# Kernel optimization log

Hardware: AMD Instinct MI355X
Metric: run time of the kernel (lower is better)

The kernel has to match this reference:

```python
import jax, jax.numpy as jnp
import numpy as np

B, C, D = 16, 128, 256


def setup_inputs() -> dict:
    key = jax.random.key(0)
    ks = jax.random.split(key, 12)
    s = 0.05
    return {
        "h_t": jax.random.normal(ks[0], (B, C, D), jnp.float32),
        "A_a": jax.random.normal(ks[1], (C, C), jnp.float32) * s,
        "A_m": jax.random.normal(ks[2], (C, C), jnp.float32) * s,
        "W1": jax.random.normal(ks[3], (2 * D, D), jnp.float32) * s,
        "b1": jax.random.normal(ks[4], (D,), jnp.float32) * s,
        "W2": jax.random.normal(ks[5], (D, 1), jnp.float32) * s,
        "b2": jax.random.normal(ks[6], (1,), jnp.float32) * s,
        "Wa": jax.random.normal(ks[7], (D, D), jnp.float32) * s,
        "ba": jax.random.normal(ks[8], (D,), jnp.float32) * s,
        "Wm": jax.random.normal(ks[9], (D, D), jnp.float32) * s,
        "bm": jax.random.normal(ks[10], (D,), jnp.float32) * s,
        "beta1": jnp.float32(1.0),
        "beta2": jnp.float32(1.0),
        "beta3": jnp.float32(1.0),
    }


def reference(h_t, A_a, A_m, W1, b1, W2, b2, Wa, ba, Wm, bm, beta1, beta2, beta3):
    d = h_t.shape[-1]
    # Pairwise edge-MLP score S[b,u,v] = sigmoid(W2 @ relu(W1 @ [h_u; h_v] + b1) + b2).
    # Split W1 into the half acting on h_u and the half acting on h_v, so the
    # (B,C,C,2D) concat never materializes (same math as Linear on the concat).
    pre_u = jnp.einsum('bud,dk->buk', h_t, W1[:d])        # (B,C,D)
    pre_v = jnp.einsum('bvd,dk->bvk', h_t, W1[d:])        # (B,C,D)
    hidden = jax.nn.relu(pre_u[:, :, None, :] + pre_v[:, None, :, :] + b1)  # (B,C,C,D)
    S = jax.nn.sigmoid(jnp.einsum('buvk,ko->buvo', hidden, W2)[..., 0] + b2[0])  # (B,C,C)

    # Additive aggregation: a_t[b,v,:] = sum_u (S*A_a)[b,u,v] * h_t[b,u,:]
    a_t = jnp.einsum('buv,bud->bvd', S * A_a, h_t)

    # Hadamard aggregation: m_t[b,v,d] = sum_u A_m[u,v] * h[b,u,d] * h[b,v,d]
    #                              = (A_m^T @ h_t) * h_t  (avoids (B,C,C,D) tensor)
    m_t = jnp.einsum('uv,bud->bvd', A_m, h_t) * h_t

    z_t = (beta1 * h_t
           + beta2 * (jnp.einsum('bvd,de->bve', a_t, Wa) + ba)
           + beta3 * (jnp.einsum('bvd,de->bve', m_t, Wm) + bm))
    return z_t
```

## Files before the change

kernel.cpp:

```cpp
#include <hip/hip_runtime.h>
#include <hip/hip_bf16.h>

#define B_ 16
#define C_ 128
#define D_ 256

typedef unsigned int uint32;
typedef unsigned short u16;
typedef __attribute__((ext_vector_type(8))) short s8v;
typedef __attribute__((ext_vector_type(4))) float f4v;

__device__ __forceinline__ u16 bfu(float x) {
  union { __hip_bfloat16 h; u16 s; } u;
  u.h = __float2bfloat16(x);
  return u.s;
}
__device__ __forceinline__ float2 bf2x(uint32 x) {
  return make_float2(__uint_as_float(x << 16), __uint_as_float(x & 0xffff0000u));
}

__global__ __launch_bounds__(256) void kprep(const float* __restrict__ h,
    const float* __restrict__ W1, const float* __restrict__ Wa,
    const float* __restrict__ Wm, const float* __restrict__ Am,
    const float* __restrict__ ba, const float* __restrict__ bm,
    const float* __restrict__ be2, const float* __restrict__ be3,
    u16* __restrict__ hbT, u16* __restrict__ w1t,
    u16* __restrict__ wcatT, u16* __restrict__ amT, float* __restrict__ bcat) {
  const int blk = blockIdx.x;
  const int tid = threadIdx.x;
  if (blk < 512) {
    const int i4 = (blk * 256 + tid) * 4;
    const int b = i4 >> 15, r = i4 & 32767, d = r >> 7, u0 = r & 127;
    ushort4 o;
    o.x = bfu(h[(b * C_ + u0 + 0) * D_ + d]);
    o.y = bfu(h[(b * C_ + u0 + 1) * D_ + d]);
    o.z = bfu(h[(b * C_ + u0 + 2) * D_ + d]);
    o.w = bfu(h[(b * C_ + u0 + 3) * D_ + d]);
    *(ushort4*)(hbT + i4) = o;
  } else if (blk < 640) {
    const int i4 = ((blk - 512) * 256 + tid) * 4;
    const int n = i4 >> 8, k0 = i4 & 255;
    float x0, x1, x2, x3;
    if (n < 256) {
      x0 = W1[(k0 + 0) * 256 + n]; x1 = W1[(k0 + 1) * 256 + n];
      x2 = W1[(k0 + 2) * 256 + n]; x3 = W1[(k0 + 3) * 256 + n];
    } else {
      const int nn = n - 256;
      x0 = W1[(256 + k0 + 0) * 256 + nn]; x1 = W1[(256 + k0 + 1) * 256 + nn];
      x2 = W1[(256 + k0 + 2) * 256 + nn]; x3 = W1[(256 + k0 + 3) * 256 + nn];
    }
    ushort4 o; o.x = bfu(x0); o.y = bfu(x1); o.z = bfu(x2); o.w = bfu(x3);
    *(ushort4*)(w1t + i4) = o;
  } else if (blk < 768) {
    const float b2v = be2[0], b3v = be3[0];
    const int i4 = ((blk - 640) * 256 + tid) * 4;
    const int n = i4 >> 9, k0 = i4 & 511;
    float x0, x1, x2, x3;
    if (k0 < 256) {
      x0 = b2v * Wa[(k0 + 0) * 256 + n]; x1 = b2v * Wa[(k0 + 1) * 256 + n];
      x2 = b2v * Wa[(k0 + 2) * 256 + n]; x3 = b2v * Wa[(k0 + 3) * 256 + n];
    } else {
      const int kk = k0 - 256;
      x0 = b3v * Wm[(kk + 0) * 256 + n]; x1 = b3v * Wm[(kk + 1) * 256 + n];
      x2 = b3v * Wm[(kk + 2) * 256 + n]; x3 = b3v * Wm[(kk + 3) * 256 + n];
    }
    ushort4 o; o.x = bfu(x0); o.y = bfu(x1); o.z = bfu(x2); o.w = bfu(x3);
    *(ushort4*)(wcatT + i4) = o;
  } else if (blk < 784) {
    const int i4 = ((blk - 768) * 256 + tid) * 4;
    const int v = i4 >> 7, u0 = i4 & 127;
    ushort4 o;
    o.x = bfu(Am[(u0 + 0) * C_ + v]);
    o.y = bfu(Am[(u0 + 1) * C_ + v]);
    o.z = bfu(Am[(u0 + 2) * C_ + v]);
    o.w = bfu(Am[(u0 + 3) * C_ + v]);
    *(ushort4*)(amT + i4) = o;
  } else {
    bcat[tid] = be2[0] * ba[tid] + be3[0] * bm[tid];
  }
}

__global__ __launch_bounds__(256) void k1_mfma(const float* __restrict__ h,
    const u16* __restrict__ w1t, const float* __restrict__ b1,
    u16* __restrict__ P, u16* __restrict__ Q) {
  const int lane = threadIdx.x & 63;
  const int w = blockIdx.x * 4 + (threadIdx.x >> 6);
  const int nt = w & 31, mt = w >> 5;
  const int row0 = mt * 16, col0 = nt * 16;
  const int lr = lane & 15, lk = lane >> 4;
  const float* ap = h + (row0 + lr) * D_ + lk * 8;
  const u16* bp = w1t + (col0 + lr) * D_ + lk * 8;
  f4v acc = {0.f, 0.f, 0.f, 0.f};
#pragma unroll
  for (int ks = 0; ks < 8; ++ks) {
    const float4 a0 = *(const float4*)(ap + ks * 32);
    const float4 a1 = *(const float4*)(ap + ks * 32 + 4);
    union { s8v v; u16 u[8]; } af;
    af.u[0] = bfu(a0.x); af.u[1] = bfu(a0.y); af.u[2] = bfu(a0.z); af.u[3] = bfu(a0.w);
    af.u[4] = bfu(a1.x); af.u[5] = bfu(a1.y); af.u[6] = bfu(a1.z); af.u[7] = bfu(a1.w);
    const s8v bf = *(const s8v*)(bp + ks * 32);
    acc = __builtin_amdgcn_mfma_f32_16x16x32_bf16(af.v, bf, acc, 0, 0, 0);
  }
  const int col = col0 + lr;
  if (col0 < 256) {
#pragma unroll
    for (int r = 0; r < 4; ++r)
      P[(row0 + lk * 4 + r) * D_ + col] = bfu(acc[r]);
  } else {
    const float bb = b1[col - 256];
#pragma unroll
    for (int r = 0; r < 4; ++r)
      Q[(row0 + lk * 4 + r) * D_ + (col - 256)] = bfu(acc[r] + bb);
  }
}

__global__ __launch_bounds__(256) void k2_s(const u16* __restrict__ P,
    const u16* __restrict__ Q, const float* __restrict__ W2,
    const float* __restrict__ b2, const float* __restrict__ Aa,
    u16* __restrict__ SA) {
  const int b = blockIdx.z;
  const int u0 = blockIdx.x * 16;
  const int v0 = blockIdx.y * 16;
  const int tid = threadIdx.x;
  __shared__ uint32 Pl[16][130];
  __shared__ uint32 Ql[16][130];
  const uint32* Pg = (const uint32*)(P + (b * C_ + u0) * D_);
  const uint32* Qg = (const uint32*)(Q + (b * C_ + v0) * D_);
  {
    const int r = tid >> 5;
    const int c4 = (tid & 31) * 4;
#pragma unroll
    for (int half = 0; half < 2; ++half) {
      const int rr = r + half * 8;
      const uint4 pv = *(const uint4*)&Pg[rr * 128 + c4];
      const uint4 qv = *(const uint4*)&Qg[rr * 128 + c4];
      *(uint2*)&Pl[rr][c4]     = make_uint2(pv.x, pv.y);
      *(uint2*)&Pl[rr][c4 + 2] = make_uint2(pv.z, pv.w);
      *(uint2*)&Ql[rr][c4]     = make_uint2(qv.x, qv.y);
      *(uint2*)&Ql[rr][c4 + 2] = make_uint2(qv.z, qv.w);
    }
  }
  __syncthreads();
  const int ul = tid & 15;
  const int vl = tid >> 4;
  const float4* __restrict__ w4 = (const float4*)W2;
  float a0 = 0.f, a1 = 0.f;
#pragma unroll 8
  for (int kk = 0; kk < 128; kk += 2) {
    const uint2 pu = *(const uint2*)&Pl[ul][kk];
    const uint2 qu = *(const uint2*)&Ql[vl][kk];
    const float4 wv = w4[kk >> 1];
    const float2 p0 = bf2x(pu.x), p1 = bf2x(pu.y);
    const float2 q0 = bf2x(qu.x), q1 = bf2x(qu.y);
    a0 = fmaf(fmaxf(p0.x + q0.x, 0.f), wv.x, a0);
    a0 = fmaf(fmaxf(p0.y + q0.y, 0.f), wv.y, a0);
    a1 = fmaf(fmaxf(p1.x + q1.x, 0.f), wv.z, a1);
    a1 = fmaf(fmaxf(p1.y + q1.y, 0.f), wv.w, a1);
  }
  const float s = 1.f / (1.f + __expf(-(a0 + a1 + b2[0])));
  const int u = u0 + ul, v = v0 + vl;
  SA[b * C_ * C_ + v * C_ + u] = bfu(s * Aa[u * C_ + v]);
}

__global__ __launch_bounds__(512) void k34_mfma(const u16* __restrict__ SA,
    const u16* __restrict__ amT, const u16* __restrict__ hbT,
    const u16* __restrict__ wcatT, const float* __restrict__ bcat,
    const float* __restrict__ h, const float* __restrict__ be1,
    float* __restrict__ z) {
  const int bid = blockIdx.x;
  const int tid = threadIdx.x;
  const int bt = bid >> 3;
  const int v0 = (bid & 7) * 16;
  const int lane = tid & 63, widx = tid >> 6;
  const int lr = lane & 15, lk = lane >> 4;
  __shared__ u16 at[16 * 512];

#pragma unroll
  for (int i = 0; i < 2; ++i) {
    const int d0 = (widx * 2 + i) * 16;
    const u16* sap = SA + (bt * C_ + v0 + lr) * C_ + lk * 8;
    const u16* a2p = amT + (v0 + lr) * C_ + lk * 8;
    const u16* bp  = hbT + (bt * D_ + d0 + lr) * C_ + lk * 8;
    f4v acca = {0.f, 0.f, 0.f, 0.f}, accm = {0.f, 0.f, 0.f, 0.f};
#pragma unroll
    for (int ks = 0; ks < 4; ++ks) {
      const s8v a1 = *(const s8v*)(sap + ks * 32);
      const s8v a2 = *(const s8v*)(a2p + ks * 32);
      const s8v bf = *(const s8v*)(bp + ks * 32);
      acca = __builtin_amdgcn_mfma_f32_16x16x32_bf16(a1, bf, acca, 0, 0, 0);
      accm = __builtin_amdgcn_mfma_f32_16x16x32_bf16(a2, bf, accm, 0, 0, 0);
    }
    const int d = d0 + lr;
#pragma unroll
    for (int r = 0; r < 4; ++r) {
      const int R = lk * 4 + r;
      const int grow = bt * C_ + v0 + R;
      const float hv = h[grow * D_ + d];
      const int swz = (R & 7) << 4;
      *(u16*)((char*)at + R * 1024 + ((d * 2) ^ swz)) = bfu(acca[r]);
      *(u16*)((char*)at + R * 1024 + (((256 + d) * 2) ^ swz)) = bfu(accm[r] * hv);
    }
  }
  __syncthreads();

  const float b1v = be1[0];
#pragma unroll
  for (int i = 0; i < 2; ++i) {
    const int col0 = (widx * 2 + i) * 16;
    const u16* bp = wcatT + (col0 + lr) * 512 + lk * 8;
    f4v acc = {0.f, 0.f, 0.f, 0.f};
#pragma unroll
    for (int ks = 0; ks < 16; ++ks) {
      const int boff = lr * 1024 + ((ks * 64 + lk * 16) ^ ((lr & 7) << 4));
      const s8v af = *(const s8v*)((char*)at + boff);
      const s8v bf = *(const s8v*)(bp + ks * 32);
      acc = __builtin_amdgcn_mfma_f32_16x16x32_bf16(af, bf, acc, 0, 0, 0);
    }
    const int col = col0 + lr;
    const float bc = bcat[col];
#pragma unroll
    for (int r = 0; r < 4; ++r) {
      const int row = bt * C_ + v0 + lk * 4 + r;
      z[row * D_ + col] = acc[r] + b1v * h[row * D_ + col] + bc;
    }
  }
}

extern "C" void kernel_launch(void* const* d_in, const int* in_sizes, int n_in,
                              void* d_out, int out_size, void* d_ws, size_t ws_size,
                              hipStream_t stream) {
  const float* h   = (const float*)d_in[0];
  const float* Aa  = (const float*)d_in[1];
  const float* Am  = (const float*)d_in[2];
  const float* W1  = (const float*)d_in[3];
  const float* b1  = (const float*)d_in[4];
  const float* W2  = (const float*)d_in[5];
  const float* b2  = (const float*)d_in[6];
  const float* Wa  = (const float*)d_in[7];
  const float* ba  = (const float*)d_in[8];
  const float* Wm  = (const float*)d_in[9];
  const float* bm  = (const float*)d_in[10];
  const float* be1 = (const float*)d_in[11];
  const float* be2 = (const float*)d_in[12];
  const float* be3 = (const float*)d_in[13];
  float* z = (float*)d_out;

  char* wsb = (char*)d_ws;
  u16*   w1t   = (u16*)(wsb);
  u16*   wcatT = (u16*)(wsb + (256 << 10));
  u16*   amT   = (u16*)(wsb + (512 << 10));
  float* bcat  = (float*)(wsb + (544 << 10));
  u16*   hbT   = (u16*)(wsb + (1 << 20));
  u16*   P     = (u16*)(wsb + (2 << 20));
  u16*   Q     = (u16*)(wsb + (3 << 20));
  u16*   SA    = (u16*)(wsb + (4 << 20));

  kprep  <<<785,  256, 0, stream>>>(h, W1, Wa, Wm, Am, ba, bm, be2, be3,
                                    hbT, w1t, wcatT, amT, bcat);
  k1_mfma<<<1024, 256, 0, stream>>>(h, w1t, b1, P, Q);
  k2_s   <<<dim3(8, 8, 16), 256, 0, stream>>>(P, Q, W2, b2, Aa, SA);
  k34_mfma<<<128, 512, 0, stream>>>(SA, amT, hbT, wcatT, bcat, h, be1, z);
}
```

Before: 122.0 us.

## Fuse edge-MLP projections into score kernel and drop weight prep kernel

Removes the separate prep and projection kernels. P and Q are now computed per tile with MFMA inside the score kernel, writing straight to shared memory, and W1, Wa, Wm, Am and h are converted from fp32 to bf16 inline rather than pre-transposed. This saves two launches and the global round-trips for the prepped weights and P/Q. In exchange, every tile recomputes its P/Q rows (8x redundancy per batch) and reads the weights with strided scalar fp32 loads, which adds heavy L2 traffic.

```diff
diff --git a/kernel.cpp b/kernel.cpp
--- a/kernel.cpp
+++ b/kernel.cpp
@@ -19,128 +19,75 @@
   return make_float2(__uint_as_float(x << 16), __uint_as_float(x & 0xffff0000u));
 }
 
-__global__ __launch_bounds__(256) void kprep(const float* __restrict__ h,
-    const float* __restrict__ W1, const float* __restrict__ Wa,
-    const float* __restrict__ Wm, const float* __restrict__ Am,
-    const float* __restrict__ ba, const float* __restrict__ bm,
-    const float* __restrict__ be2, const float* __restrict__ be3,
-    u16* __restrict__ hbT, u16* __restrict__ w1t,
-    u16* __restrict__ wcatT, u16* __restrict__ amT, float* __restrict__ bcat) {
-  const int blk = blockIdx.x;
-  const int tid = threadIdx.x;
-  if (blk < 512) {
-    const int i4 = (blk * 256 + tid) * 4;
-    const int b = i4 >> 15, r = i4 & 32767, d = r >> 7, u0 = r & 127;
-    ushort4 o;
-    o.x = bfu(h[(b * C_ + u0 + 0) * D_ + d]);
-    o.y = bfu(h[(b * C_ + u0 + 1) * D_ + d]);
-    o.z = bfu(h[(b * C_ + u0 + 2) * D_ + d]);
-    o.w = bfu(h[(b * C_ + u0 + 3) * D_ + d]);
-    *(ushort4*)(hbT + i4) = o;
-  } else if (blk < 640) {
-    const int i4 = ((blk - 512) * 256 + tid) * 4;
-    const int n = i4 >> 8, k0 = i4 & 255;
-    float x0, x1, x2, x3;
-    if (n < 256) {
-      x0 = W1[(k0 + 0) * 256 + n]; x1 = W1[(k0 + 1) * 256 + n];
-      x2 = W1[(k0 + 2) * 256 + n]; x3 = W1[(k0 + 3) * 256 + n];
-    } else {
-      const int nn = n - 256;
-      x0 = W1[(256 + k0 + 0) * 256 + nn]; x1 = W1[(256 + k0 + 1) * 256 + nn];
-      x2 = W1[(256 + k0 + 2) * 256 + nn]; x3 = W1[(256 + k0 + 3) * 256 + nn];
-    }
-    ushort4 o; o.x = bfu(x0); o.y = bfu(x1); o.z = bfu(x2); o.w = bfu(x3);
-    *(ushort4*)(w1t + i4) = o;
-  } else if (blk < 768) {
-    const float b2v = be2[0], b3v = be3[0];
-    const int i4 = ((blk - 640) * 256 + tid) * 4;
-    const int n = i4 >> 9, k0 = i4 & 511;
-    float x0, x1, x2, x3;
-    if (k0 < 256) {
-      x0 = b2v * Wa[(k0 + 0) * 256 + n]; x1 = b2v * Wa[(k0 + 1) * 256 + n];
-      x2 = b2v * Wa[(k0 + 2) * 256 + n]; x3 = b2v * Wa[(k0 + 3) * 256 + n];
-    } else {
-      const int kk = k0 - 256;
-      x0 = b3v * Wm[(kk + 0) * 256 + n]; x1 = b3v * Wm[(kk + 1) * 256 + n];
-      x2 = b3v * Wm[(kk + 2) * 256 + n]; x3 = b3v * Wm[(kk + 3) * 256 + n];
-    }
-    ushort4 o; o.x = bfu(x0); o.y = bfu(x1); o.z = bfu(x2); o.w = bfu(x3);
-    *(ushort4*)(wcatT + i4) = o;
-  } else if (blk < 784) {
-    const int i4 = ((blk - 768) * 256 + tid) * 4;
-    const int v = i4 >> 7, u0 = i4 & 127;
-    ushort4 o;
-    o.x = bfu(Am[(u0 + 0) * C_ + v]);
-    o.y = bfu(Am[(u0 + 1) * C_ + v]);
-    o.z = bfu(Am[(u0 + 2) * C_ + v]);
-    o.w = bfu(Am[(u0 + 3) * C_ + v]);
-    *(ushort4*)(amT + i4) = o;
-  } else {
-    bcat[tid] = be2[0] * ba[tid] + be3[0] * bm[tid];
-  }
-}
-
-__global__ __launch_bounds__(256) void k1_mfma(const float* __restrict__ h,
-    const u16* __restrict__ w1t, const float* __restrict__ b1,
-    u16* __restrict__ P, u16* __restrict__ Q) {
-  const int lane = threadIdx.x & 63;
-  const int w = blockIdx.x * 4 + (threadIdx.x >> 6);
-  const int nt = w & 31, mt = w >> 5;
-  const int row0 = mt * 16, col0 = nt * 16;
-  const int lr = lane & 15, lk = lane >> 4;
-  const float* ap = h + (row0 + lr) * D_ + lk * 8;
-  const u16* bp = w1t + (col0 + lr) * D_ + lk * 8;
-  f4v acc = {0.f, 0.f, 0.f, 0.f};
-#pragma unroll
-  for (int ks = 0; ks < 8; ++ks) {
-    const float4 a0 = *(const float4*)(ap + ks * 32);
-    const float4 a1 = *(const float4*)(ap + ks * 32 + 4);
-    union { s8v v; u16 u[8]; } af;
-    af.u[0] = bfu(a0.x); af.u[1] = bfu(a0.y); af.u[2] = bfu(a0.z); af.u[3] = bfu(a0.w);
-    af.u[4] = bfu(a1.x); af.u[5] = bfu(a1.y); af.u[6] = bfu(a1.z); af.u[7] = bfu(a1.w);
-    const s8v bf = *(const s8v*)(bp + ks * 32);
-    acc = __builtin_amdgcn_mfma_f32_16x16x32_bf16(af.v, bf, acc, 0, 0, 0);
-  }
-  const int col = col0 + lr;
-  if (col0 < 256) {
-#pragma unroll
-    for (int r = 0; r < 4; ++r)
-      P[(row0 + lk * 4 + r) * D_ + col] = bfu(acc[r]);
-  } else {
-    const float bb = b1[col - 256];
-#pragma unroll
-    for (int r = 0; r < 4; ++r)
-      Q[(row0 + lk * 4 + r) * D_ + (col - 256)] = bfu(acc[r] + bb);
-  }
-}
-
-__global__ __launch_bounds__(256) void k2_s(const u16* __restrict__ P,
-    const u16* __restrict__ Q, const float* __restrict__ W2,
-    const float* __restrict__ b2, const float* __restrict__ Aa,
-    u16* __restrict__ SA) {
+__global__ __launch_bounds__(256) void k12(const float* __restrict__ h,
+    const float* __restrict__ W1, const float* __restrict__ b1,
+    const float* __restrict__ W2, const float* __restrict__ b2,
+    const float* __restrict__ Aa, u16* __restrict__ SA) {
   const int b = blockIdx.z;
   const int u0 = blockIdx.x * 16;
   const int v0 = blockIdx.y * 16;
   const int tid = threadIdx.x;
+  const int lane = tid & 63;
+  const int widx = tid >> 6;
+  const int lr = lane & 15, lk = lane >> 4;
   __shared__ uint32 Pl[16][130];
   __shared__ uint32 Ql[16][130];
-  const uint32* Pg = (const uint32*)(P + (b * C_ + u0) * D_);
-  const uint32* Qg = (const uint32*)(Q + (b * C_ + v0) * D_);
-  {
-    const int r = tid >> 5;
-    const int c4 = (tid & 31) * 4;
-#pragma unroll
-    for (int half = 0; half < 2; ++half) {
-      const int rr = r + half * 8;
-      const uint4 pv = *(const uint4*)&Pg[rr * 128 + c4];
-      const uint4 qv = *(const uint4*)&Qg[rr * 128 + c4];
-      *(uint2*)&Pl[rr][c4]     = make_uint2(pv.x, pv.y);
-      *(uint2*)&Pl[rr][c4 + 2] = make_uint2(pv.z, pv.w);
-      *(uint2*)&Ql[rr][c4]     = make_uint2(qv.x, qv.y);
-      *(uint2*)&Ql[rr][c4 + 2] = make_uint2(qv.z, qv.w);
-    }
+  u16* PlH = (u16*)&Pl[0][0];
+  u16* QlH = (u16*)&Ql[0][0];
+
+  const float* apP = h + (b * C_ + u0 + lr) * D_ + lk * 8;
+  const float* apQ = h + (b * C_ + v0 + lr) * D_ + lk * 8;
+  s8v aP[8], aQ[8];
+#pragma unroll
+  for (int ks = 0; ks < 8; ++ks) {
+    const float4 x0 = *(const float4*)(apP + ks * 32);
+    const float4 x1 = *(const float4*)(apP + ks * 32 + 4);
+    const float4 y0 = *(const float4*)(apQ + ks * 32);
+    const float4 y1 = *(const float4*)(apQ + ks * 32 + 4);
+    union { s8v v; u16 u[8]; } t, s;
+    t.u[0] = bfu(x0.x); t.u[1] = bfu(x0.y); t.u[2] = bfu(x0.z); t.u[3] = bfu(x0.w);
+    t.u[4] = bfu(x1.x); t.u[5] = bfu(x1.y); t.u[6] = bfu(x1.z); t.u[7] = bfu(x1.w);
+    s.u[0] = bfu(y0.x); s.u[1] = bfu(y0.y); s.u[2] = bfu(y0.z); s.u[3] = bfu(y0.w);
+    s.u[4] = bfu(y1.x); s.u[5] = bfu(y1.y); s.u[6] = bfu(y1.z); s.u[7] = bfu(y1.w);
+    aP[ks] = t.v;
+    aQ[ks] = s.v;
+  }
+
+#pragma unroll
+  for (int i = 0; i < 4; ++i) {
+    const int n = (widx * 4 + i) * 16 + lr;
+    f4v acc = {0.f, 0.f, 0.f, 0.f};
+#pragma unroll
+    for (int ks = 0; ks < 8; ++ks) {
+      union { s8v v; u16 u[8]; } bf;
+#pragma unroll
+      for (int j = 0; j < 8; ++j)
+        bf.u[j] = bfu(W1[(ks * 32 + lk * 8 + j) * D_ + n]);
+      acc = __builtin_amdgcn_mfma_f32_16x16x32_bf16(aP[ks], bf.v, acc, 0, 0, 0);
+    }
+#pragma unroll
+    for (int r = 0; r < 4; ++r)
+      PlH[(lk * 4 + r) * 260 + n] = bfu(acc[r]);
+  }
+#pragma unroll
+  for (int i = 0; i < 4; ++i) {
+    const int n = (widx * 4 + i) * 16 + lr;
+    f4v acc = {0.f, 0.f, 0.f, 0.f};
+#pragma unroll
+    for (int ks = 0; ks < 8; ++ks) {
+      union { s8v v; u16 u[8]; } bf;
+#pragma unroll
+      for (int j = 0; j < 8; ++j)
+        bf.u[j] = bfu(W1[(D_ + ks * 32 + lk * 8 + j) * D_ + n]);
+      acc = __builtin_amdgcn_mfma_f32_16x16x32_bf16(aQ[ks], bf.v, acc, 0, 0, 0);
+    }
+    const float bb = b1[n];
+#pragma unroll
+    for (int r = 0; r < 4; ++r)
+      QlH[(lk * 4 + r) * 260 + n] = bfu(acc[r] + bb);
   }
   __syncthreads();
+
   const int ul = tid & 15;
   const int vl = tid >> 4;
   const float4* __restrict__ w4 = (const float4*)W2;
@@ -162,11 +109,12 @@
   SA[b * C_ * C_ + v * C_ + u] = bfu(s * Aa[u * C_ + v]);
 }
 
-__global__ __launch_bounds__(512) void k34_mfma(const u16* __restrict__ SA,
-    const u16* __restrict__ amT, const u16* __restrict__ hbT,
-    const u16* __restrict__ wcatT, const float* __restrict__ bcat,
-    const float* __restrict__ h, const float* __restrict__ be1,
-    float* __restrict__ z) {
+__global__ __launch_bounds__(512) void k34(const u16* __restrict__ SA,
+    const float* __restrict__ Am, const float* __restrict__ h,
+    const float* __restrict__ Wa, const float* __restrict__ Wm,
+    const float* __restrict__ ba, const float* __restrict__ bm,
+    const float* __restrict__ be1, const float* __restrict__ be2,
+    const float* __restrict__ be3, float* __restrict__ z) {
   const int bid = blockIdx.x;
   const int tid = threadIdx.x;
   const int bt = bid >> 3;
@@ -174,23 +122,27 @@
   const int lane = tid & 63, widx = tid >> 6;
   const int lr = lane & 15, lk = lane >> 4;
   __shared__ u16 at[16 * 512];
+  const float b2v = be2[0], b3v = be3[0];
 
 #pragma unroll
   for (int i = 0; i < 2; ++i) {
     const int d0 = (widx * 2 + i) * 16;
+    const int d = d0 + lr;
     const u16* sap = SA + (bt * C_ + v0 + lr) * C_ + lk * 8;
-    const u16* a2p = amT + (v0 + lr) * C_ + lk * 8;
-    const u16* bp  = hbT + (bt * D_ + d0 + lr) * C_ + lk * 8;
     f4v acca = {0.f, 0.f, 0.f, 0.f}, accm = {0.f, 0.f, 0.f, 0.f};
 #pragma unroll
     for (int ks = 0; ks < 4; ++ks) {
       const s8v a1 = *(const s8v*)(sap + ks * 32);
-      const s8v a2 = *(const s8v*)(a2p + ks * 32);
-      const s8v bf = *(const s8v*)(bp + ks * 32);
-      acca = __builtin_amdgcn_mfma_f32_16x16x32_bf16(a1, bf, acca, 0, 0, 0);
-      accm = __builtin_amdgcn_mfma_f32_16x16x32_bf16(a2, bf, accm, 0, 0, 0);
-    }
-    const int d = d0 + lr;
+      union { s8v v; u16 u[8]; } a2, bf;
+#pragma unroll
+      for (int j = 0; j < 8; ++j) {
+        const int uu = ks * 32 + lk * 8 + j;
+        a2.u[j] = bfu(Am[uu * C_ + v0 + lr]);
+        bf.u[j] = bfu(h[(bt * C_ + uu) * D_ + d]);
+      }
+      acca = __builtin_amdgcn_mfma_f32_16x16x32_bf16(a1, bf.v, acca, 0, 0, 0);
+      accm = __builtin_amdgcn_mfma_f32_16x16x32_bf16(a2.v, bf.v, accm, 0, 0, 0);
+    }
 #pragma unroll
     for (int r = 0; r < 4; ++r) {
       const int R = lk * 4 + r;
@@ -206,18 +158,29 @@
   const float b1v = be1[0];
 #pragma unroll
   for (int i = 0; i < 2; ++i) {
-    const int col0 = (widx * 2 + i) * 16;
-    const u16* bp = wcatT + (col0 + lr) * 512 + lk * 8;
+    const int col = (widx * 2 + i) * 16 + lr;
     f4v acc = {0.f, 0.f, 0.f, 0.f};
 #pragma unroll
-    for (int ks = 0; ks < 16; ++ks) {
+    for (int ks = 0; ks < 8; ++ks) {
       const int boff = lr * 1024 + ((ks * 64 + lk * 16) ^ ((lr & 7) << 4));
       const s8v af = *(const s8v*)((char*)at + boff);
-      const s8v bf = *(const s8v*)(bp + ks * 32);
-      acc = __builtin_amdgcn_mfma_f32_16x16x32_bf16(af, bf, acc, 0, 0, 0);
-    }
-    const int col = col0 + lr;
-    const float bc = bcat[col];
+      union { s8v v; u16 u[8]; } bf;
+#pragma unroll
+      for (int j = 0; j < 8; ++j)
+        bf.u[j] = bfu(b2v * Wa[(ks * 32 + lk * 8 + j) * D_ + col]);
+      acc = __builtin_amdgcn_mfma_f32_16x16x32_bf16(af, bf.v, acc, 0, 0, 0);
+    }
+#pragma unroll
+    for (int ks = 8; ks < 16; ++ks) {
+      const int boff = lr * 1024 + ((ks * 64 + lk * 16) ^ ((lr & 7) << 4));
+      const s8v af = *(const s8v*)((char*)at + boff);
+      union { s8v v; u16 u[8]; } bf;
+#pragma unroll
+      for (int j = 0; j < 8; ++j)
+        bf.u[j] = bfu(b3v * Wm[((ks - 8) * 32 + lk * 8 + j) * D_ + col]);
+      acc = __builtin_amdgcn_mfma_f32_16x16x32_bf16(af, bf.v, acc, 0, 0, 0);
+    }
+    const float bc = b2v * ba[col] + b3v * bm[col];
 #pragma unroll
     for (int r = 0; r < 4; ++r) {
       const int row = bt * C_ + v0 + lk * 4 + r;
@@ -245,19 +208,8 @@
   const float* be3 = (const float*)d_in[13];
   float* z = (float*)d_out;
 
-  char* wsb = (char*)d_ws;
-  u16*   w1t   = (u16*)(wsb);
-  u16*   wcatT = (u16*)(wsb + (256 << 10));
-  u16*   amT   = (u16*)(wsb + (512 << 10));
-  float* bcat  = (float*)(wsb + (544 << 10));
-  u16*   hbT   = (u16*)(wsb + (1 << 20));
-  u16*   P     = (u16*)(wsb + (2 << 20));
-  u16*   Q     = (u16*)(wsb + (3 << 20));
-  u16*   SA    = (u16*)(wsb + (4 << 20));
-
-  kprep  <<<785,  256, 0, stream>>>(h, W1, Wa, Wm, Am, ba, bm, be2, be3,
-                                    hbT, w1t, wcatT, amT, bcat);
-  k1_mfma<<<1024, 256, 0, stream>>>(h, w1t, b1, P, Q);
-  k2_s   <<<dim3(8, 8, 16), 256, 0, stream>>>(P, Q, W2, b2, Aa, SA);
-  k34_mfma<<<128, 512, 0, stream>>>(SA, amT, hbT, wcatT, bcat, h, be1, z);
-}
+  u16* SA = (u16*)d_ws;
+
+  k12<<<dim3(8, 8, 16), 256, 0, stream>>>(h, W1, b1, W2, b2, Aa, SA);
+  k34<<<128, 512, 0, stream>>>(SA, Am, h, Wa, Wm, ba, bm, be1, be2, be3, z);
+}
```

New measurement: 142.7 us. 1.17x slower.
